# Performance work log

Hardware: AMD Instinct MI355X
Metric: run time of the kernel (lower is better)

Reference implementation:

```python
import jax, jax.numpy as jnp
import numpy as np

N_QUBIT = 20
N_LAYER = 50
FEAT = 128
BATCH = 128
N_NODES = BATCH * N_QUBIT * (N_LAYER + 1)  # 130560
N_EDGES = 524288
VOCAB = N_QUBIT * (N_LAYER + 1) + 1  # 1021
NEG_SLOPE = 0.01


def setup_inputs() -> dict:
    key = jax.random.key(0)
    ks = jax.random.split(key, 32)
    s = 0.05
    x = jax.random.randint(ks[0], (N_NODES,), 0, VOCAB, dtype=jnp.int64 if jax.config.read('jax_enable_x64') else jnp.int32)
    edge_index = jax.random.randint(ks[1], (2, N_EDGES), 0, N_NODES, dtype=x.dtype)
    emb = (jax.random.normal(ks[2], (VOCAB, FEAT), jnp.float32) * s).at[0].set(0.0)  # padding_idx=0
    gcn_w = jax.random.normal(ks[3], (5, FEAT, FEAT), jnp.float32) * s
    gcn_b = jnp.zeros((5, FEAT), jnp.float32)
    mlp_dims = [(2 * FEAT, 2 * FEAT), (2 * FEAT, FEAT), (FEAT, FEAT), (FEAT, FEAT // 2), (FEAT // 2, FEAT // 2), (FEAT // 2, 1)]
    mlp = {}
    for i, (din, dout) in enumerate(mlp_dims):
        mlp[f'mw{i}'] = jax.random.normal(ks[4 + i], (din, dout), jnp.float32) * s
        mlp[f'mb{i}'] = jnp.zeros((dout,), jnp.float32)
    return dict(x=x, edge_index=edge_index, emb=emb, gcn_w=gcn_w, gcn_b=gcn_b, **mlp)


def _leaky(v):
    return jnp.where(v >= 0, v, NEG_SLOPE * v)


def _gcn(h, src, dst, W, b):
    # PyG GCNConv: h' = D^-1/2 (A+I) D^-1/2 (h W) + b, flow src -> dst
    n = h.shape[0]
    hw = h @ W
    loops = jnp.arange(n, dtype=src.dtype)
    s2 = jnp.concatenate([src, loops])
    d2 = jnp.concatenate([dst, loops])
    deg = jax.ops.segment_sum(jnp.ones(s2.shape[0], hw.dtype), d2, num_segments=n)
    dinv = jnp.where(deg > 0, jax.lax.rsqrt(deg), 0.0)
    norm = dinv[s2] * dinv[d2]  # [E+N]
    out = jax.ops.segment_sum(hw[s2] * norm[:, None], d2, num_segments=n)
    return out + b


def reference(x, edge_index, emb, gcn_w, gcn_b, mw0, mb0, mw1, mb1, mw2, mb2, mw3, mb3, mw4, mb4, mw5, mb5):
    src, dst = edge_index[0], edge_index[1]
    h = emb[x]  # [N, f]
    for i in range(4):
        h = _leaky(_gcn(h, src, dst, gcn_w[i], gcn_b[i])) + h
    h = _gcn(h, src, dst, gcn_w[4], gcn_b[4]) + h
    n, f = N_QUBIT, FEAT
    h = h.reshape(-1, n * (N_LAYER + 1), f)[:, :n, :]  # [B, n, f]
    b = h.shape[0]
    # cartesian pairs (i, j): concat(h_i, h_j) -> [B, n, n, 2f]
    xi = jnp.broadcast_to(h[:, :, None, :], (b, n, n, f))
    xj = jnp.broadcast_to(h[:, None, :, :], (b, n, n, f))
    p = jnp.concatenate([xi, xj], axis=-1)
    p = _leaky(p @ mw0 + mb0)
    p = _leaky(p @ mw1 + mb1)
    p = _leaky(p @ mw2 + mb2)
    p = _leaky(p @ mw3 + mb3)
    p = _leaky(p @ mw4 + mb4)
    p = (p @ mw5 + mb5)[..., 0]  # [B, n, n]
    p = (p + jnp.swapaxes(p, -1, -2)) / 2
    return p.reshape(-1, n * n)
```

## Files before the change

kernel.cpp:

```cpp
#include <hip/hip_runtime.h>
#include <hip/hip_bf16.h>

#define NQ 20
#define NLAY 51
#define FEAT 128
#define BATCH 128
#define NN (BATCH * NQ * NLAY)
#define NE 524288
#define NPAIR (BATCH * NQ * NQ)
#define NB (NN / 256)
#define VOCAB 1021

typedef _Float16 half8 __attribute__((ext_vector_type(8)));
typedef float floatx4 __attribute__((ext_vector_type(4)));
typedef unsigned int uint;

__device__ __forceinline__ float lrelu(float v) { return v >= 0.f ? v : 0.01f * v; }

__device__ __forceinline__ uint packhl(float v) {
    _Float16 h = (_Float16)v;
    _Float16 l = (_Float16)(v - (float)h);
    union { _Float16 f; unsigned short u; } hb, lb;
    hb.f = h; lb.f = l;
    return (uint)hb.u | ((uint)lb.u << 16);
// ... 17 lines not shown
    int e = blockIdx.x * 256 + threadIdx.x;
    atomicAdd(&cnt[dst[e]], 1);
}

__global__ void k_offsets(const int* __restrict__ cnt, const int* __restrict__ x,
                          int* __restrict__ offs, float* __restrict__ dinv,
                          int4* __restrict__ meta, int* __restrict__ cursor,
                          int* __restrict__ flag1, int* __restrict__ idmap) {
    __shared__ int sm[256];
    __shared__ int sbase;
    int t = threadIdx.x, g = blockIdx.x * 256 + t;
    int v = cnt[g];
    sm[t] = v;
    __syncthreads();
    for (int s = 1; s < 256; s <<= 1) {
        int add = (t >= s) ? sm[t - s] : 0;
        __syncthreads();
        sm[t] += add;
        __syncthreads();
    }
    if (t == 255) sbase = atomicAdd(cursor, sm[255]);
    __syncthreads();
    int off = sbase + sm[t] - v;
    float di = rsqrtf((float)(v + 1));
    offs[g] = off;
    dinv[g] = di;
    meta[g] = make_int4(off, v, __float_as_int(di), x[g]);
    if (g % (NQ * NLAY) < NQ) flag1[g] = 1;
    if (g < 1024) idmap[g] = min(g, VOCAB - 1);
}

__global__ void k_fill(const int* __restrict__ src, const int* __restrict__ dst,
                       const int* __restrict__ offs, int* __restrict__ fill,
                       const float* __restrict__ dinv, const int* __restrict__ x,
                       int2* __restrict__ csre, int2* __restrict__ csre0,
                       int* __restrict__ flag1) {
    int e = blockIdx.x * 256 + threadIdx.x;
    int d = dst[e];
    int s = src[e];
    int pos = offs[d] + atomicAdd(&fill[d], 1);
    int wb = __float_as_int(dinv[s] * dinv[d]);
    csre[pos] = make_int2(s, wb);
    csre0[pos] = make_int2(x[s], wb);
    if (d % (NQ * NLAY) < NQ) flag1[s] = 1;
}

__global__ void k_s1pass(const int* __restrict__ flagI, const int4* __restrict__ meta,
                         const int2* __restrict__ csre, int* __restrict__ cur,
                         int* __restrict__ listO, int4* __restrict__ recO,
                         int* __restrict__ flagO) {
    __shared__ int sm[256];
    __shared__ int sbase;
    int t = threadIdx.x, g = blockIdx.x * 256 + t;
    int v = flagI[g];
    sm[t] = v;
    __syncthreads();
    for (int s = 1; s < 256; s <<= 1) {
        int add = (t >= s) ? sm[t - s] : 0;
        __syncthreads();
        sm[t] += add;
        __syncthreads();
    }
    if (t == 255) sbase = atomicAdd(cur, sm[255]);
    __syncthreads();
    if (v) {
        int slot = sbase + sm[t] - 1;
        listO[slot] = g;
        int4 m = meta[g];
        float di = __int_as_float(m.z);
        int dc = min(m.y, 6);
        int2 eb[6];
#pragma unroll
        for (int j = 0; j < 6; j++) eb[j] = (j < dc) ? csre[m.x + j] : make_int2(0, 0);
        int4* r = recO + (size_t)slot * 4;
        r[0] = make_int4(g + 1, m.y, __float_as_int(di * di), m.x);
        r[1] = make_int4(eb[0].x, eb[0].y, eb[1].x, eb[1].y);
        r[2] = make_int4(eb[2].x, eb[2].y, eb[3].x, eb[3].y);
        r[3] = make_int4(eb[4].x, eb[4].y, eb[5].x, eb[5].y);
        if (flagO) {
            flagO[g] = 1;
            for (int e = 0; e < m.y; e++) flagO[csre[m.x + e].x] = 1;
        }
    }
}

#define OFF_GCN 0
#define OFF_P0  81920
#define OFF_M1  147456
#define OFF_M2  180224
#define OFF_M3  196608
#define OFF_M4  204800
#define TS_TOTAL 208896

__global__ void k_tsplit_all(const float* __restrict__ gw, const float* __restrict__ mw0,
                             const float* __restrict__ mw1, const float* __restrict__ mw2,
                             const float* __restrict__ mw3, const float* __restrict__ mw4,
                             _Float16* __restrict__ hi, _Float16* __restrict__ lo) {
    int idx = blockIdx.x * 256 + threadIdx.x;
    const float* src;
    int K, N, rel;
    bool p0 = false;
    if (idx < OFF_P0) {
        int L = (idx - OFF_GCN) >> 14; rel = (idx - OFF_GCN) & 16383;
        src = gw + L * 16384; K = 128; N = 128;
    } else if (idx < OFF_M1) {
        rel = idx - OFF_P0; src = mw0; K = 128; N = 512; p0 = true;
    } else if (idx < OFF_M2) {
        rel = idx - OFF_M1;  src = mw1; K = 256; N = 128;
    } else if (idx < OFF_M3) {
        rel = idx - OFF_M2;  src = mw2; K = 128; N = 128;
    } else if (idx < OFF_M4) {
        rel = idx - OFF_M3;  src = mw3; K = 128; N = 64;
    } else {
        rel = idx - OFF_M4;  src = mw4; K = 64;  N = 64;
    }
    int kblks = K >> 5;
    int j = rel & 7;
    int lane = (rel >> 3) & 63;
    int t2 = rel >> 9;
    int kblk = t2 % kblks;
    int ntile = t2 / kblks;
    int col = ntile * 16 + (lane & 15);
    int k = kblk * 32 + ((lane >> 4) << 3) + j;
    float f;
    if (p0) {
        f = (col < 256) ? src[k * 256 + col] : src[(k + 128) * 256 + (col - 256)];
    } else {
        f = src[k * N + col];
    }
    _Float16 h = (_Float16)f;
    hi[idx] = h;
    lo[idx] = (_Float16)(f - (float)h);
}

template <int NT_N, bool LEAKY, bool BIAS, bool P0SPLIT, bool FUSEA, bool GATHA, bool LISTM>
__launch_bounds__(256, 2)
__global__ void hgemm(const float* __restrict__ A,
                      const float* __restrict__ FA, const float* __restrict__ FB,
                      const _Float16* __restrict__ Bh, const _Float16* __restrict__ Bl,
                      const float* __restrict__ bias,
                      float* __restrict__ C, float* __restrict__ C2,
                      int N, int K, const int* __restrict__ gmap,
                      const int* __restrict__ listm) {
    if (LISTM) {
        if ((unsigned)listm[blockIdx.x * 128] >= (unsigned)NN) return;
    }
    const int KB = K >> 5;
    const int lane = threadIdx.x & 63;
    const int wid = threadIdx.x >> 6;
    const int lm = lane & 15, lq = lane >> 4;
    const int m0 = blockIdx.x * 128 + wid * 32;
    const int n0t = blockIdx.y * NT_N;

    const float* arow[2];
    const float* brow[2];
#pragma unroll
    for (int mt = 0; mt < 2; mt++) {
        int row = m0 + mt * 16 + lm;
        if (FUSEA) {
            int b = row / (NQ * NQ);
            int rr = row - b * (NQ * NQ);
            int i = rr / NQ;
            int j = rr - i * NQ;
            arow[mt] = FA + (size_t)(b * NQ + i) * 256;
            brow[mt] = FB + (size_t)(b * NQ + j) * 256;
        } else if (GATHA) {
// ... 14 lines not shown
        for (int nt = 0; nt < NT_N; nt++) acc[mt][nt] = (floatx4)0.f;

    for (int kb = 0; kb < KB; kb++) {
        const int k0 = kb * 32 + lq * 8;
        half8 ahi[2], alo[2];
#pragma unroll
        for (int mt = 0; mt < 2; mt++) {
            floatx4 av0, av1;
            if (FUSEA) {
                floatx4 fa0 = *(const floatx4*)(arow[mt] + k0);
                floatx4 fa1 = *(const floatx4*)(arow[mt] + k0 + 4);
                floatx4 fb0 = *(const floatx4*)(brow[mt] + k0);
                floatx4 fb1 = *(const floatx4*)(brow[mt] + k0 + 4);
#pragma unroll
                for (int q = 0; q < 4; q++) {
                    av0[q] = lrelu(fa0[q] + fb0[q]);
                    av1[q] = lrelu(fa1[q] + fb1[q]);
                }
            } else {
                av0 = *(const floatx4*)(arow[mt] + k0);
                av1 = *(const floatx4*)(arow[mt] + k0 + 4);
            }
#pragma unroll
            for (int q = 0; q < 4; q++) {
                _Float16 h0 = (_Float16)av0[q];
                ahi[mt][q] = h0;
                alo[mt][q] = (_Float16)(av0[q] - (float)h0);
                _Float16 h1 = (_Float16)av1[q];
                ahi[mt][4 + q] = h1;
                alo[mt][4 + q] = (_Float16)(av1[q] - (float)h1);
            }
        }
#pragma unroll
        for (int nt = 0; nt < NT_N; nt++) {
            size_t boff = (((size_t)(n0t + nt) * KB + kb) * 64 + lane) * 8;
            half8 bhi = *(const half8*)(Bh + boff);
            half8 blo = *(const half8*)(Bl + boff);
#pragma unroll
            for (int mt = 0; mt < 2; mt++) {
                acc[mt][nt] = __builtin_amdgcn_mfma_f32_16x16x32_f16(ahi[mt], bhi, acc[mt][nt], 0, 0, 0);
                acc[mt][nt] = __builtin_amdgcn_mfma_f32_16x16x32_f16(ahi[mt], blo, acc[mt][nt], 0, 0, 0);
                acc[mt][nt] = __builtin_amdgcn_mfma_f32_16x16x32_f16(alo[mt], bhi, acc[mt][nt], 0, 0, 0);
            }
        }
    }

    int strow[2][4];
    bool svalid[2][4];
#pragma unroll
    for (int mt = 0; mt < 2; mt++)
#pragma unroll
        for (int r = 0; r < 4; r++) {
            int mlog = m0 + mt * 16 + lq * 4 + r;
            if (LISTM) {
                int sr = listm[mlog];
                svalid[mt][r] = (unsigned)sr < (unsigned)NN;
                strow[mt][r] = svalid[mt][r] ? sr : 0;
            } else {
                svalid[mt][r] = true;
                strow[mt][r] = mlog;
            }
        }

#pragma unroll
    for (int nt = 0; nt < NT_N; nt++) {
        int col = (n0t + nt) * 16 + lm;
        float bv = (BIAS || P0SPLIT) ? bias[col < 256 ? col : 0] : 0.f;
#pragma unroll
        for (int mt = 0; mt < 2; mt++) {
#pragma unroll
            for (int r = 0; r < 4; r++) {
                if (!svalid[mt][r]) continue;
                int row = strow[mt][r];
                float val = acc[mt][nt][r];
                if (P0SPLIT) {
                    if (col < 256) C[(size_t)row * 256 + col] = val + bv;
                    else C2[(size_t)row * 256 + col - 256] = val;
                } else {
                    if (BIAS) val += bv;
                    if (LEAKY) val = lrelu(val);
                    C[(size_t)row * N + col] = val;
                }
            }
        }
    }
}

template <int KB, int NT>
__device__ __forceinline__ void pair_stage(uint (*__restrict__ X)[132],
                                           const _Float16* __restrict__ Bh,
                                           const _Float16* __restrict__ Bl,
                                           const float* __restrict__ bias,
                                           int srow, int lane) {
    const int lm = lane & 15, lq = lane >> 4;
    floatx4 acc[NT];
#pragma unroll
    for (int nt = 0; nt < NT; nt++) acc[nt] = (floatx4)0.f;
#pragma unroll
    for (int kb = 0; kb < KB; kb++) {
        const int k0 = kb * 32 + lq * 8;
        uint4 pa = *(const uint4*)&X[srow + lm][k0];
        uint4 pb = *(const uint4*)&X[srow + lm][k0 + 4];
        half8 ahi, alo;
        unpack8(pa, pb, ahi, alo);
#pragma unroll
        for (int nt = 0; nt < NT; nt++) {
            size_t boff = (((size_t)nt * KB + kb) * 64 + lane) * 8;
            half8 bhi = *(const half8*)(Bh + boff);
            half8 blo = *(const half8*)(Bl + boff);
            acc[nt] = __builtin_amdgcn_mfma_f32_16x16x32_f16(ahi, bhi, acc[nt], 0, 0, 0);
            acc[nt] = __builtin_amdgcn_mfma_f32_16x16x32_f16(ahi, blo, acc[nt], 0, 0, 0);
            acc[nt] = __builtin_amdgcn_mfma_f32_16x16x32_f16(alo, bhi, acc[nt], 0, 0, 0);
        }
    }
#pragma unroll
    for (int nt = 0; nt < NT; nt++) {
        int col = nt * 16 + lm;
        float bv = bias[col];
#pragma unroll
        for (int r = 0; r < 4; r++) {
            X[srow + lq * 4 + r][col] = packhl(lrelu(acc[nt][r] + bv));
        }
    }
}

__launch_bounds__(256, 4)
__global__ void k_pair(const float* __restrict__ FA, const float* __restrict__ FB,
                       const _Float16* __restrict__ bth, const _Float16* __restrict__ btl,
                       const float* __restrict__ mb1, const float* __restrict__ mb2,
                       const float* __restrict__ mb3, const float* __restrict__ mb4,
                       const float* __restrict__ mw5, const float* __restrict__ mb5,
                       float* __restrict__ sbuf) {
    __shared__ uint X[64][132];
    const int lane = threadIdx.x & 63;
    const int wid = threadIdx.x >> 6;
    const int lm = lane & 15, lq = lane >> 4;
    const int srow = wid * 16;
    const int rbase = blockIdx.x * 64;

    {
        const int grow = rbase + srow + lm;
        int b = grow / (NQ * NQ);
        int rr = grow - b * (NQ * NQ);
        int i = rr / NQ;
        int j = rr - i * NQ;
        const float* arow = FA + (size_t)(b * NQ + i) * 256;
        const float* brow = FB + (size_t)(b * NQ + j) * 256;
        const _Float16* Bh = bth + OFF_M1;
        const _Float16* Bl = btl + OFF_M1;
        floatx4 acc[8];
#pragma unroll
        for (int nt = 0; nt < 8; nt++) acc[nt] = (floatx4)0.f;
        const int KB = 8;
#pragma unroll
        for (int kb = 0; kb < KB; kb++) {
            const int k0 = kb * 32 + lq * 8;
            floatx4 fa0 = *(const floatx4*)(arow + k0);
            floatx4 fa1 = *(const floatx4*)(arow + k0 + 4);
            floatx4 fb0 = *(const floatx4*)(brow + k0);
            floatx4 fb1 = *(const floatx4*)(brow + k0 + 4);
            half8 ahi, alo;
#pragma unroll
            for (int q = 0; q < 4; q++) {
                float v0 = lrelu(fa0[q] + fb0[q]);
                float v1 = lrelu(fa1[q] + fb1[q]);
                _Float16 h0 = (_Float16)v0;
// ... 49 lines not shown
        if (part == 0) sbuf[rbase + row] = s + mb5[0];
    }
}

__global__ void k_sym(const float* __restrict__ sbuf, float* __restrict__ out) {
    int p = blockIdx.x * 256 + threadIdx.x;
    int b = p / (NQ * NQ);
    int rr = p - b * (NQ * NQ);
    int i = rr / NQ, j = rr - i * NQ;
    float a = sbuf[p];
    float c = sbuf[b * (NQ * NQ) + j * NQ + i];
    out[p] = 0.5f * (a + c);
}

__global__ void k_agg0(const float* __restrict__ embW, const float* __restrict__ emb,
                       float* __restrict__ h,
                       const int4* __restrict__ meta, const int2* __restrict__ csre0,
                       const float* __restrict__ bias) {
    int tid = threadIdx.x;
    int sl = tid & 31;
    int p = blockIdx.x * 8 + (tid >> 5);
    int n0 = p * 2, n1 = n0 + 1;
    int4 m0 = meta[n0], m1 = meta[n1];
    float di0 = __int_as_float(m0.z), di1 = __int_as_float(m1.z);
    int off0 = m0.x, deg0 = m0.y;
    int off1 = m1.x, deg1 = m1.y;
    float4 v0 = ((const float4*)(embW + (size_t)m0.w * FEAT))[sl];
    float4 v1 = ((const float4*)(embW + (size_t)m1.w * FEAT))[sl];
    float4 ho0 = ((const float4*)(emb + (size_t)m0.w * FEAT))[sl];
    float4 ho1 = ((const float4*)(emb + (size_t)m1.w * FEAT))[sl];
    float s20 = di0 * di0, s21 = di1 * di1;
    float a0x = v0.x * s20, a0y = v0.y * s20, a0z = v0.z * s20, a0w = v0.w * s20;
    float a1x = v1.x * s21, a1y = v1.y * s21, a1z = v1.z * s21, a1w = v1.w * s21;
    int d0c = max(deg0 - 1, 0), d1c = max(deg1 - 1, 0);
    int dm = max(deg0, deg1);
    for (int e = 0; e < dm; e += 4) {
        int2 e00 = csre0[off0 + min(e,     d0c)];
        int2 e01 = csre0[off0 + min(e + 1, d0c)];
        int2 e02 = csre0[off0 + min(e + 2, d0c)];
        int2 e03 = csre0[off0 + min(e + 3, d0c)];
        int2 e10 = csre0[off1 + min(e,     d1c)];
        int2 e11 = csre0[off1 + min(e + 1, d1c)];
        int2 e12 = csre0[off1 + min(e + 2, d1c)];
        int2 e13 = csre0[off1 + min(e + 3, d1c)];
        float4 u00 = ((const float4*)(embW + (size_t)e00.x * FEAT))[sl];
        float4 u01 = ((const float4*)(embW + (size_t)e01.x * FEAT))[sl];
        float4 u02 = ((const float4*)(embW + (size_t)e02.x * FEAT))[sl];
        float4 u03 = ((const float4*)(embW + (size_t)e03.x * FEAT))[sl];
        float4 u10 = ((const float4*)(embW + (size_t)e10.x * FEAT))[sl];
        float4 u11 = ((const float4*)(embW + (size_t)e11.x * FEAT))[sl];
        float4 u12 = ((const float4*)(embW + (size_t)e12.x * FEAT))[sl];
        float4 u13 = ((const float4*)(embW + (size_t)e13.x * FEAT))[sl];
        float w00 = (e     < deg0) ? __int_as_float(e00.y) : 0.f;
        float w01 = (e + 1 < deg0) ? __int_as_float(e01.y) : 0.f;
        float w02 = (e + 2 < deg0) ? __int_as_float(e02.y) : 0.f;
        float w03 = (e + 3 < deg0) ? __int_as_float(e03.y) : 0.f;
        float w10 = (e     < deg1) ? __int_as_float(e10.y) : 0.f;
        float w11 = (e + 1 < deg1) ? __int_as_float(e11.y) : 0.f;
        float w12 = (e + 2 < deg1) ? __int_as_float(e12.y) : 0.f;
        float w13 = (e + 3 < deg1) ? __int_as_float(e13.y) : 0.f;
        a0x += u00.x * w00 + u01.x * w01 + u02.x * w02 + u03.x * w03;
        a0y += u00.y * w00 + u01.y * w01 + u02.y * w02 + u03.y * w03;
        a0z += u00.z * w00 + u01.z * w01 + u02.z * w02 + u03.z * w03;
        a0w += u00.w * w00 + u01.w * w01 + u02.w * w02 + u03.w * w03;
        a1x += u10.x * w10 + u11.x * w11 + u12.x * w12 + u13.x * w13;
        a1y += u10.y * w10 + u11.y * w11 + u12.y * w12 + u13.y * w13;
        a1z += u10.z * w10 + u11.z * w11 + u12.z * w12 + u13.z * w13;
        a1w += u10.w * w10 + u11.w * w11 + u12.w * w12 + u13.w * w13;
    }
    float4 bv = ((const float4*)bias)[sl];
    float4 r0, r1;
    r0.x = lrelu(a0x + bv.x) + ho0.x;
    r0.y = lrelu(a0y + bv.y) + ho0.y;
    r0.z = lrelu(a0z + bv.z) + ho0.z;
    r0.w = lrelu(a0w + bv.w) + ho0.w;
    r1.x = lrelu(a1x + bv.x) + ho1.x;
    r1.y = lrelu(a1y + bv.y) + ho1.y;
    r1.z = lrelu(a1z + bv.z) + ho1.z;
    r1.w = lrelu(a1w + bv.w) + ho1.w;
    ((float4*)(h + (size_t)n0 * FEAT))[sl] = r0;
    ((float4*)(h + (size_t)n1 * FEAT))[sl] = r1;
}

__global__ void k_agg(const float* __restrict__ hw, float* __restrict__ h,
                      const int4* __restrict__ rec, const int2* __restrict__ csre,
                      const int* __restrict__ cntp, const float* __restrict__ bias) {
    int lcnt = *cntp;
    if (blockIdx.x * 16 >= lcnt) return;
    int tid = threadIdx.x;
    int sl = tid & 31;
    int p = blockIdx.x * 8 + (tid >> 5);
    int p0i = p * 2, p1i = p0i + 1;
    bool val0 = p0i < lcnt, val1 = p1i < lcnt;
    const int4* r0p = rec + (size_t)(val0 ? p0i : 0) * 4;
    const int4* r1p = rec + (size_t)(val1 ? p1i : 0) * 4;
    int4 hd0 = r0p[0], ea0 = r0p[1], eb0 = r0p[2], ec0 = r0p[3];
    int4 hd1 = r1p[0], ea1 = r1p[1], eb1 = r1p[2], ec1 = r1p[3];
    int n0 = hd0.x - 1;
    int n1 = hd1.x - 1;
    float s20 = __int_as_float(hd0.z), s21 = __int_as_float(hd1.z);
    const float4* hw4 = (const float4*)hw;
    float4 v0  = hw4[(size_t)n0 * 32 + sl];
    float4 v1  = hw4[(size_t)n1 * 32 + sl];
    float4 u00 = hw4[(size_t)ea0.x * 32 + sl];
    float4 u01 = hw4[(size_t)ea0.z * 32 + sl];
    float4 u02 = hw4[(size_t)eb0.x * 32 + sl];
    float4 u03 = hw4[(size_t)eb0.z * 32 + sl];
    float4 u04 = hw4[(size_t)ec0.x * 32 + sl];
    float4 u05 = hw4[(size_t)ec0.z * 32 + sl];
    float4 u10 = hw4[(size_t)ea1.x * 32 + sl];
    float4 u11 = hw4[(size_t)ea1.z * 32 + sl];
    float4 u12 = hw4[(size_t)eb1.x * 32 + sl];
    float4 u13 = hw4[(size_t)eb1.z * 32 + sl];
    float4 u14 = hw4[(size_t)ec1.x * 32 + sl];
    float4 u15 = hw4[(size_t)ec1.z * 32 + sl];
    float4 ho0 = ((const float4*)h)[(size_t)n0 * 32 + sl];
    float4 ho1 = ((const float4*)h)[(size_t)n1 * 32 + sl];
    float w00 = __int_as_float(ea0.y), w01 = __int_as_float(ea0.w);
    float w02 = __int_as_float(eb0.y), w03 = __int_as_float(eb0.w);
    float w04 = __int_as_float(ec0.y), w05 = __int_as_float(ec0.w);
    float w10 = __int_as_float(ea1.y), w11 = __int_as_float(ea1.w);
    float w12 = __int_as_float(eb1.y), w13 = __int_as_float(eb1.w);
    float w14 = __int_as_float(ec1.y), w15 = __int_as_float(ec1.w);
    float a0x = v0.x * s20 + u00.x * w00 + u01.x * w01 + u02.x * w02 + u03.x * w03 + u04.x * w04 + u05.x * w05;
    float a0y = v0.y * s20 + u00.y * w00 + u01.y * w01 + u02.y * w02 + u03.y * w03 + u04.y * w04 + u05.y * w05;
    float a0z = v0.z * s20 + u00.z * w00 + u01.z * w01 + u02.z * w02 + u03.z * w03 + u04.z * w04 + u05.z * w05;
    float a0w = v0.w * s20 + u00.w * w00 + u01.w * w01 + u02.w * w02 + u03.w * w03 + u04.w * w04 + u05.w * w05;
    float a1x = v1.x * s21 + u10.x * w10 + u11.x * w11 + u12.x * w12 + u13.x * w13 + u14.x * w14 + u15.x * w15;
    float a1y = v1.y * s21 + u10.y * w10 + u11.y * w11 + u12.y * w12 + u13.y * w13 + u14.y * w14 + u15.y * w15;
    float a1z = v1.z * s21 + u10.z * w10 + u11.z * w11 + u12.z * w12 + u13.z * w13 + u14.z * w14 + u15.z * w15;
    float a1w = v1.w * s21 + u10.w * w10 + u11.w * w11 + u12.w * w12 + u13.w * w13 + u14.w * w14 + u15.w * w15;
    int deg0 = val0 ? hd0.y : 0, deg1 = val1 ? hd1.y : 0;
    int dm = max(deg0, deg1);
    if (dm > 6) {
        int off0 = hd0.w, off1 = hd1.w;
        int d0c = max(deg0 - 1, 0), d1c = max(deg1 - 1, 0);
        for (int e = 6; e < dm; e += 6) {
            int2 e00 = csre[off0 + min(e,     d0c)];
            int2 e01 = csre[off0 + min(e + 1, d0c)];
            int2 e02 = csre[off0 + min(e + 2, d0c)];
            int2 e03 = csre[off0 + min(e + 3, d0c)];
            int2 e04 = csre[off0 + min(e + 4, d0c)];
            int2 e05 = csre[off0 + min(e + 5, d0c)];
            int2 e10 = csre[off1 + min(e,     d1c)];
            int2 e11 = csre[off1 + min(e + 1, d1c)];
            int2 e12 = csre[off1 + min(e + 2, d1c)];
            int2 e13 = csre[off1 + min(e + 3, d1c)];
            int2 e14 = csre[off1 + min(e + 4, d1c)];
            int2 e15 = csre[off1 + min(e + 5, d1c)];
            float4 x00 = hw4[(size_t)e00.x * 32 + sl];
            float4 x01 = hw4[(size_t)e01.x * 32 + sl];
            float4 x02 = hw4[(size_t)e02.x * 32 + sl];
            float4 x03 = hw4[(size_t)e03.x * 32 + sl];
            float4 x04 = hw4[(size_t)e04.x * 32 + sl];
            float4 x05 = hw4[(size_t)e05.x * 32 + sl];
            float4 x10 = hw4[(size_t)e10.x * 32 + sl];
            float4 x11 = hw4[(size_t)e11.x * 32 + sl];
            float4 x12 = hw4[(size_t)e12.x * 32 + sl];
            float4 x13 = hw4[(size_t)e13.x * 32 + sl];
            float4 x14 = hw4[(size_t)e14.x * 32 + sl];
            float4 x15 = hw4[(size_t)e15.x * 32 + sl];
            float q00 = (e     < deg0) ? __int_as_float(e00.y) : 0.f;
            float q01 = (e + 1 < deg0) ? __int_as_float(e01.y) : 0.f;
            float q02 = (e + 2 < deg0) ? __int_as_float(e02.y) : 0.f;
            float q03 = (e + 3 < deg0) ? __int_as_float(e03.y) : 0.f;
            float q04 = (e + 4 < deg0) ? __int_as_float(e04.y) : 0.f;
            float q05 = (e + 5 < deg0) ? __int_as_float(e05.y) : 0.f;
            float q10 = (e     < deg1) ? __int_as_float(e10.y) : 0.f;
            float q11 = (e + 1 < deg1) ? __int_as_float(e11.y) : 0.f;
            float q12 = (e + 2 < deg1) ? __int_as_float(e12.y) : 0.f;
            float q13 = (e + 3 < deg1) ? __int_as_float(e13.y) : 0.f;
            float q14 = (e + 4 < deg1) ? __int_as_float(e14.y) : 0.f;
            float q15 = (e + 5 < deg1) ? __int_as_float(e15.y) : 0.f;
            a0x += x00.x * q00 + x01.x * q01 + x02.x * q02 + x03.x * q03 + x04.x * q04 + x05.x * q05;
            a0y += x00.y * q00 + x01.y * q01 + x02.y * q02 + x03.y * q03 + x04.y * q04 + x05.y * q05;
            a0z += x00.z * q00 + x01.z * q01 + x02.z * q02 + x03.z * q03 + x04.z * q04 + x05.z * q05;
            a0w += x00.w * q00 + x01.w * q01 + x02.w * q02 + x03.w * q03 + x04.w * q04 + x05.w * q05;
            a1x += x10.x * q10 + x11.x * q11 + x12.x * q12 + x13.x * q13 + x14.x * q14 + x15.x * q15;
            a1y += x10.y * q10 + x11.y * q11 + x12.y * q12 + x13.y * q13 + x14.y * q14 + x15.y * q15;
            a1z += x10.z * q10 + x11.z * q11 + x12.z * q12 + x13.z * q13 + x14.z * q14 + x15.z * q15;
            a1w += x10.w * q10 + x11.w * q11 + x12.w * q12 + x13.w * q13 + x14.w * q14 + x15.w * q15;
        }
    }
    float4 bv = ((const float4*)bias)[sl];
    float4 r0, r1;
    r0.x = lrelu(a0x + bv.x) + ho0.x;
    r0.y = lrelu(a0y + bv.y) + ho0.y;
    r0.z = lrelu(a0z + bv.z) + ho0.z;
    r0.w = lrelu(a0w + bv.w) + ho0.w;
    r1.x = lrelu(a1x + bv.x) + ho1.x;
    r1.y = lrelu(a1y + bv.y) + ho1.y;
    r1.z = lrelu(a1z + bv.z) + ho1.z;
    r1.w = lrelu(a1w + bv.w) + ho1.w;
    if (val0) ((float4*)(h + (size_t)n0 * FEAT))[sl] = r0;
    if (val1) ((float4*)(h + (size_t)n1 * FEAT))[sl] = r1;
}

__global__ void k_aggq(const float* __restrict__ hw, const float* __restrict__ h,
                       const int4* __restrict__ meta, const int2* __restrict__ csre,
                       const float* __restrict__ gbias, float* __restrict__ hq) {
    int tid = threadIdx.x;
    int sl = tid & 31;
    int q = blockIdx.x * 8 + (tid >> 5);
    int b = q / NQ, i = q - b * NQ;
    int node = b * (NQ * NLAY) + i;
    int4 m = meta[node];
    float di = __int_as_float(m.z);
    int off = m.x, deg = m.y;
    float s2 = di * di;
    float4 v = ((const float4*)(hw + (size_t)node * FEAT))[sl];
    float ax = v.x * s2, ay = v.y * s2, az = v.z * s2, aw = v.w * s2;
    int dc = max(deg - 1, 0);
    for (int e = 0; e < deg; e += 4) {
        int2 e0 = csre[off + min(e,     dc)];
        int2 e1 = csre[off + min(e + 1, dc)];
        int2 e2 = csre[off + min(e + 2, dc)];
        int2 e3 = csre[off + min(e + 3, dc)];
        float4 u0 = ((const float4*)(hw + (size_t)e0.x * FEAT))[sl];
        float4 u1 = ((const float4*)(hw + (size_t)e1.x * FEAT))[sl];
        float4 u2 = ((const float4*)(hw + (size_t)e2.x * FEAT))[sl];
        float4 u3 = ((const float4*)(hw + (size_t)e3.x * FEAT))[sl];
        float w0 = (e     < deg) ? __int_as_float(e0.y) : 0.f;
        float w1 = (e + 1 < deg) ? __int_as_float(e1.y) : 0.f;
        float w2 = (e + 2 < deg) ? __int_as_float(e2.y) : 0.f;
        float w3 = (e + 3 < deg) ? __int_as_float(e3.y) : 0.f;
        ax += u0.x * w0 + u1.x * w1 + u2.x * w2 + u3.x * w3;
        ay += u0.y * w0 + u1.y * w1 + u2.y * w2 + u3.y * w3;
        az += u0.z * w0 + u1.z * w1 + u2.z * w2 + u3.z * w3;
        aw += u0.w * w0 + u1.w * w1 + u2.w * w2 + u3.w * w3;
    }
    float4 bv = ((const float4*)gbias)[sl];
    float4 ho = ((const float4*)(h + (size_t)node * FEAT))[sl];
    ((float4*)(hq + (size_t)q * FEAT))[sl] =
        make_float4(ax + bv.x + ho.x, ay + bv.y + ho.y, az + bv.z + ho.z, aw + bv.w + ho.w);
}

extern "C" void kernel_launch(void* const* d_in, const int* in_sizes, int n_in,
                              void* d_out, int out_size, void* d_ws, size_t ws_size,
                              hipStream_t stream) {
    const int* x = (const int*)d_in[0];
    const int* ei = (const int*)d_in[1];
    const int* e_src = ei;
    const int* e_dst = ei + NE;
    const float* emb = (const float*)d_in[2];
    const float* gw = (const float*)d_in[3];
    const float* gb = (const float*)d_in[4];
    const float* mw0 = (const float*)d_in[5];
    const float* mb0 = (const float*)d_in[6];
    const float* mw1 = (const float*)d_in[7];
    const float* mb1 = (const float*)d_in[8];
    const float* mw2 = (const float*)d_in[9];
    const float* mb2 = (const float*)d_in[10];
    const float* mw3 = (const float*)d_in[11];
    const float* mb3 = (const float*)d_in[12];
    const float* mw4 = (const float*)d_in[13];
    const float* mb4 = (const float*)d_in[14];
    const float* mw5 = (const float*)d_in[15];
    const float* mb5 = (const float*)d_in[16];
    float* out = (float*)d_out;

    float* wsf = (float*)d_ws;
    size_t o = 0;
    const size_t HSZ = (size_t)NN * FEAT;
    float* h  = wsf + o; o += HSZ;
    float* hw = wsf + o; o += HSZ;
    int* cnt   = (int*)(wsf + o); o += NN;
    int* fill  = (int*)(wsf + o); o += NN;
    int* flag1 = (int*)(wsf + o); o += NN;
    int* flag2 = (int*)(wsf + o); o += NN;
    int* flag3 = (int*)(wsf + o); o += NN;
    int* curs  = (int*)(wsf + o); o += 16;
    int* list1 = (int*)(wsf + o); o += NN;
    int* list2 = (int*)(wsf + o); o += NN;
    int* list3 = (int*)(wsf + o); o += NN;
    int* offs = (int*)(wsf + o); o += NN;
    float* dinv = wsf + o; o += NN;
    int4* meta = (int4*)(wsf + o); o += 4 * (size_t)NN;
    int2* csre  = (int2*)(wsf + o); o += 2 * (size_t)(NE + 8);
    int2* csre0 = (int2*)(wsf + o); o += 2 * (size_t)(NE + 8);
    int* idmap = (int*)(wsf + o); o += 1024;
    float* embW = wsf + o; o += (size_t)1024 * FEAT;
    float* hq = wsf + o; o += (size_t)BATCH * NQ * FEAT;
    float* Abuf = wsf + o; o += (size_t)BATCH * NQ * 256;
    float* Bbuf = wsf + o; o += (size_t)BATCH * NQ * 256;
    int4* rec1 = (int4*)(wsf + o); o += 16 * (size_t)NN;
    int4* rec2 = (int4*)(wsf + o); o += 16 * (size_t)NN;
    int4* rec3 = (int4*)(wsf + o); o += 16 * (size_t)NN;
    _Float16* bt_hi = (_Float16*)(wsf + o); o += (TS_TOTAL + 2) / 2;
    _Float16* bt_lo = (_Float16*)(wsf + o); o += (TS_TOTAL + 2) / 2;
    float* sbuf = hw;

    k_tsplit_all<<<TS_TOTAL / 256, 256, 0, stream>>>(gw, mw0, mw1, mw2, mw3, mw4, bt_hi, bt_lo);

    hipMemsetAsync(cnt, 0, (5 * NN + 16) * sizeof(int), stream);
    hipMemsetAsync(list1, 0xFF, 3 * NN * sizeof(int), stream);
    hipMemsetAsync(csre + NE, 0, 8 * sizeof(int2), stream);
    hipMemsetAsync(csre0 + NE, 0, 8 * sizeof(int2), stream);
    k_count<<<NE / 256, 256, 0, stream>>>(e_dst, cnt);
    k_offsets<<<NB, 256, 0, stream>>>(cnt, x, offs, dinv, meta, curs + 0, flag1, idmap);
    k_fill<<<NE / 256, 256, 0, stream>>>(e_src, e_dst, offs, fill, dinv, x, csre, csre0, flag1);
    k_s1pass<<<NB, 256, 0, stream>>>(flag1, meta, csre, curs + 1, list1, rec1, flag2);
    k_s1pass<<<NB, 256, 0, stream>>>(flag2, meta, csre, curs + 2, list2, rec2, flag3);
    k_s1pass<<<NB, 256, 0, stream>>>(flag3, meta, csre, curs + 3, list3, rec3, nullptr);

    hgemm<1, false, false, false, false, true, false><<<dim3(8, 8), 256, 0, stream>>>(
        emb, nullptr, nullptr, bt_hi + OFF_GCN, bt_lo + OFF_GCN,
        nullptr, embW, nullptr, FEAT, FEAT, idmap, nullptr);
    k_agg0<<<NN / 16, 256, 0, stream>>>(embW, emb, h, meta, csre0, gb + 0 * FEAT);

    hgemm<8, false, false, false, false, false, false><<<dim3(NN / 128, 1), 256, 0, stream>>>(
        h, nullptr, nullptr, bt_hi + OFF_GCN + 1 * 16384, bt_lo + OFF_GCN + 1 * 16384,
        nullptr, hw, nullptr, FEAT, FEAT, nullptr, nullptr);
    k_agg<<<NN / 16, 256, 0, stream>>>(hw, h, rec3, csre, curs + 3, gb + 1 * FEAT);

    hgemm<8, false, false, false, false, false, true><<<dim3(NN / 128, 1), 256, 0, stream>>>(
        h, nullptr, nullptr, bt_hi + OFF_GCN + 2 * 16384, bt_lo + OFF_GCN + 2 * 16384,
        nullptr, hw, nullptr, FEAT, FEAT, nullptr, list3);
    k_agg<<<NN / 16, 256, 0, stream>>>(hw, h, rec2, csre, curs + 2, gb + 2 * FEAT);

    hgemm<8, false, false, false, false, false, true><<<dim3(NN / 128, 1), 256, 0, stream>>>(
        h, nullptr, nullptr, bt_hi + OFF_GCN + 3 * 16384, bt_lo + OFF_GCN + 3 * 16384,
        nullptr, hw, nullptr, FEAT, FEAT, nullptr, list2);
    k_agg<<<NN / 16, 256, 0, stream>>>(hw, h, rec1, csre, curs + 1, gb + 3 * FEAT);

    hgemm<8, false, false, false, false, false, true><<<dim3(NN / 128, 1), 256, 0, stream>>>(
        h, nullptr, nullptr, bt_hi + OFF_GCN + 4 * 16384, bt_lo + OFF_GCN + 4 * 16384,
        nullptr, hw, nullptr, FEAT, FEAT, nullptr, list1);
    k_aggq<<<(BATCH * NQ) / 8, 256, 0, stream>>>(hw, h, meta, csre,
                                                 gb + 4 * (size_t)FEAT, hq);

    hgemm<2, false, false, true, false, false, false><<<dim3(20, 16), 256, 0, stream>>>(
        hq, nullptr, nullptr, bt_hi + OFF_P0, bt_lo + OFF_P0, mb0, Abuf, Bbuf, 512, 128,
        nullptr, nullptr);
    k_pair<<<NPAIR / 64, 256, 0, stream>>>(Abuf, Bbuf, bt_hi, bt_lo,
                                           mb1, mb2, mb3, mb4, mw5, mb5, sbuf);
    k_sym<<<NPAIR / 256, 256, 0, stream>>>(sbuf, out);
}
```

Measured before the change: 470.5 us.

## Fuse GCN aggregation with weight GEMM by aggregating features before transform

Reorders each GCN layer from A·(H·W) to (A·H)·W. The normalized neighbor aggregation is gathered directly into a shared-memory tile of split-fp16 values, and the 128x128 weight multiply is then done with MFMA in the same kernel. Bias, leaky ReLU and the residual add are applied in the epilogue, and h/hw act as ping-pong buffers. The separate per-layer hgemm launches, the full-size hw intermediate round trip and the list memset are removed, and a small rec0 record table drives the final query-node layer. In exchange each block does gathers and a GEMM together, which uses more LDS and registers and may lower occupancy.

```diff
diff --git a/kernel.cpp b/kernel.cpp
--- a/kernel.cpp
+++ b/kernel.cpp
@@ -123,6 +123,25 @@
             for (int e = 0; e < m.y; e++) flagO[csre[m.x + e].x] = 1;
         }
     }
+}
+
+__global__ void k_rec0(const int4* __restrict__ meta, const int2* __restrict__ csre,
+                       int4* __restrict__ rec0) {
+    int q = blockIdx.x * 256 + threadIdx.x;
+    if (q >= BATCH * NQ) return;
+    int b = q / NQ, i = q - b * NQ;
+    int node = b * (NQ * NLAY) + i;
+    int4 m = meta[node];
+    float di = __int_as_float(m.z);
+    int dc = min(m.y, 6);
+    int2 eb[6];
+#pragma unroll
+    for (int j = 0; j < 6; j++) eb[j] = (j < dc) ? csre[m.x + j] : make_int2(0, 0);
+    int4* r = rec0 + (size_t)q * 4;
+    r[0] = make_int4(node + 1, m.y, __float_as_int(di * di), m.x);
+    r[1] = make_int4(eb[0].x, eb[0].y, eb[1].x, eb[1].y);
+    r[2] = make_int4(eb[2].x, eb[2].y, eb[3].x, eb[3].y);
+    r[3] = make_int4(eb[4].x, eb[4].y, eb[5].x, eb[5].y);
 }
 
 #define OFF_GCN 0
@@ -303,6 +322,169 @@
                     C[(size_t)row * N + col] = val;
                 }
             }
+        }
+    }
+}
+
+template <bool LEAKY, bool FINAL>
+__launch_bounds__(256, 4)
+__global__ void k_lagg(const float* __restrict__ in, float* __restrict__ outp,
+                       const int4* __restrict__ rec, const int2* __restrict__ csre,
+                       const int* __restrict__ cntp, int fixcnt,
+                       const _Float16* __restrict__ Bh, const _Float16* __restrict__ Bl,
+                       const float* __restrict__ bias) {
+    int lcnt = cntp ? *cntp : fixcnt;
+    int sbase = blockIdx.x * 64;
+    if (sbase >= lcnt) return;
+    __shared__ uint X[64][132];
+    int tid = threadIdx.x;
+    int sl = tid & 31;
+    int grp = tid >> 5;
+    const float4* in4 = (const float4*)in;
+#pragma unroll 1
+    for (int pass = 0; pass < 4; pass++) {
+        int lrow0 = pass * 16 + grp * 2;
+        int p0i = sbase + lrow0, p1i = p0i + 1;
+        bool val0 = p0i < lcnt, val1 = p1i < lcnt;
+        const int4* r0p = rec + (size_t)(val0 ? p0i : 0) * 4;
+        const int4* r1p = rec + (size_t)(val1 ? p1i : 0) * 4;
+        int4 hd0 = r0p[0], ea0 = r0p[1], eb0 = r0p[2], ec0 = r0p[3];
+        int4 hd1 = r1p[0], ea1 = r1p[1], eb1 = r1p[2], ec1 = r1p[3];
+        int n0 = hd0.x - 1;
+        int n1 = hd1.x - 1;
+        float s20 = __int_as_float(hd0.z), s21 = __int_as_float(hd1.z);
+        float4 v0  = in4[(size_t)n0 * 32 + sl];
+        float4 v1  = in4[(size_t)n1 * 32 + sl];
+        float4 u00 = in4[(size_t)ea0.x * 32 + sl];
+        float4 u01 = in4[(size_t)ea0.z * 32 + sl];
+        float4 u02 = in4[(size_t)eb0.x * 32 + sl];
+        float4 u03 = in4[(size_t)eb0.z * 32 + sl];
+        float4 u04 = in4[(size_t)ec0.x * 32 + sl];
+        float4 u05 = in4[(size_t)ec0.z * 32 + sl];
+        float4 u10 = in4[(size_t)ea1.x * 32 + sl];
+        float4 u11 = in4[(size_t)ea1.z * 32 + sl];
+        float4 u12 = in4[(size_t)eb1.x * 32 + sl];
+        float4 u13 = in4[(size_t)eb1.z * 32 + sl];
+        float4 u14 = in4[(size_t)ec1.x * 32 + sl];
+        float4 u15 = in4[(size_t)ec1.z * 32 + sl];
+        float w00 = __int_as_float(ea0.y), w01 = __int_as_float(ea0.w);
+        float w02 = __int_as_float(eb0.y), w03 = __int_as_float(eb0.w);
+        float w04 = __int_as_float(ec0.y), w05 = __int_as_float(ec0.w);
+        float w10 = __int_as_float(ea1.y), w11 = __int_as_float(ea1.w);
+        float w12 = __int_as_float(eb1.y), w13 = __int_as_float(eb1.w);
+        float w14 = __int_as_float(ec1.y), w15 = __int_as_float(ec1.w);
+        float a0x = v0.x * s20 + u00.x * w00 + u01.x * w01 + u02.x * w02 + u03.x * w03 + u04.x * w04 + u05.x * w05;
+        float a0y = v0.y * s20 + u00.y * w00 + u01.y * w01 + u02.y * w02 + u03.y * w03 + u04.y * w04 + u05.y * w05;
+        float a0z = v0.z * s20 + u00.z * w00 + u01.z * w01 + u02.z * w02 + u03.z * w03 + u04.z * w04 + u05.z * w05;
+        float a0w = v0.w * s20 + u00.w * w00 + u01.w * w01 + u02.w * w02 + u03.w * w03 + u04.w * w04 + u05.w * w05;
+        float a1x = v1.x * s21 + u10.x * w10 + u11.x * w11 + u12.x * w12 + u13.x * w13 + u14.x * w14 + u15.x * w15;
+        float a1y = v1.y * s21 + u10.y * w10 + u11.y * w11 + u12.y * w12 + u13.y * w13 + u14.y * w14 + u15.y * w15;
+        float a1z = v1.z * s21 + u10.z * w10 + u11.z * w11 + u12.z * w12 + u13.z * w13 + u14.z * w14 + u15.z * w15;
+        float a1w = v1.w * s21 + u10.w * w10 + u11.w * w11 + u12.w * w12 + u13.w * w13 + u14.w * w14 + u15.w * w15;
+        int deg0 = val0 ? hd0.y : 0, deg1 = val1 ? hd1.y : 0;
+        int dm = max(deg0, deg1);
+        if (dm > 6) {
+            int off0 = hd0.w, off1 = hd1.w;
+            int d0c = max(deg0 - 1, 0), d1c = max(deg1 - 1, 0);
+            for (int e = 6; e < dm; e += 6) {
+                int2 e00 = csre[off0 + min(e,     d0c)];
+                int2 e01 = csre[off0 + min(e + 1, d0c)];
+                int2 e02 = csre[off0 + min(e + 2, d0c)];
+                int2 e03 = csre[off0 + min(e + 3, d0c)];
+                int2 e04 = csre[off0 + min(e + 4, d0c)];
+                int2 e05 = csre[off0 + min(e + 5, d0c)];
+                int2 e10 = csre[off1 + min(e,     d1c)];
+                int2 e11 = csre[off1 + min(e + 1, d1c)];
+                int2 e12 = csre[off1 + min(e + 2, d1c)];
+                int2 e13 = csre[off1 + min(e + 3, d1c)];
+                int2 e14 = csre[off1 + min(e + 4, d1c)];
+                int2 e15 = csre[off1 + min(e + 5, d1c)];
+                float4 x00 = in4[(size_t)e00.x * 32 + sl];
+                float4 x01 = in4[(size_t)e01.x * 32 + sl];
+                float4 x02 = in4[(size_t)e02.x * 32 + sl];
+                float4 x03 = in4[(size_t)e03.x * 32 + sl];
+                float4 x04 = in4[(size_t)e04.x * 32 + sl];
+                float4 x05 = in4[(size_t)e05.x * 32 + sl];
+                float4 x10 = in4[(size_t)e10.x * 32 + sl];
+                float4 x11 = in4[(size_t)e11.x * 32 + sl];
+                float4 x12 = in4[(size_t)e12.x * 32 + sl];
+                float4 x13 = in4[(size_t)e13.x * 32 + sl];
+                float4 x14 = in4[(size_t)e14.x * 32 + sl];
+                float4 x15 = in4[(size_t)e15.x * 32 + sl];
+                float q00 = (e     < deg0) ? __int_as_float(e00.y) : 0.f;
+                float q01 = (e + 1 < deg0) ? __int_as_float(e01.y) : 0.f;
+                float q02 = (e + 2 < deg0) ? __int_as_float(e02.y) : 0.f;
+                float q03 = (e + 3 < deg0) ? __int_as_float(e03.y) : 0.f;
+                float q04 = (e + 4 < deg0) ? __int_as_float(e04.y) : 0.f;
+                float q05 = (e + 5 < deg0) ? __int_as_float(e05.y) : 0.f;
+                float q10 = (e     < deg1) ? __int_as_float(e10.y) : 0.f;
+                float q11 = (e + 1 < deg1) ? __int_as_float(e11.y) : 0.f;
+                float q12 = (e + 2 < deg1) ? __int_as_float(e12.y) : 0.f;
+                float q13 = (e + 3 < deg1) ? __int_as_float(e13.y) : 0.f;
+                float q14 = (e + 4 < deg1) ? __int_as_float(e14.y) : 0.f;
+                float q15 = (e + 5 < deg1) ? __int_as_float(e15.y) : 0.f;
+                a0x += x00.x * q00 + x01.x * q01 + x02.x * q02 + x03.x * q03 + x04.x * q04 + x05.x * q05;
+                a0y += x00.y * q00 + x01.y * q01 + x02.y * q02 + x03.y * q03 + x04.y * q04 + x05.y * q05;
+                a0z += x00.z * q00 + x01.z * q01 + x02.z * q02 + x03.z * q03 + x04.z * q04 + x05.z * q05;
+                a0w += x00.w * q00 + x01.w * q01 + x02.w * q02 + x03.w * q03 + x04.w * q04 + x05.w * q05;
+                a1x += x10.x * q10 + x11.x * q11 + x12.x * q12 + x13.x * q13 + x14.x * q14 + x15.x * q15;
+                a1y += x10.y * q10 + x11.y * q11 + x12.y * q12 + x13.y * q13 + x14.y * q14 + x15.y * q15;
+                a1z += x10.z * q10 + x11.z * q11 + x12.z * q12 + x13.z * q13 + x14.z * q14 + x15.z * q15;
+                a1w += x10.w * q10 + x11.w * q11 + x12.w * q12 + x13.w * q13 + x14.w * q14 + x15.w * q15;
+            }
+        }
+        *(uint4*)&X[lrow0][sl * 4] =
+            make_uint4(packhl(a0x), packhl(a0y), packhl(a0z), packhl(a0w));
+        *(uint4*)&X[lrow0 + 1][sl * 4] =
+            make_uint4(packhl(a1x), packhl(a1y), packhl(a1z), packhl(a1w));
+    }
+    __syncthreads();
+    const int lane = tid & 63;
+    const int wid = tid >> 6;
+    const int lm = lane & 15, lq = lane >> 4;
+    const int srow = wid * 16;
+    floatx4 acc[8];
+#pragma unroll
+    for (int nt = 0; nt < 8; nt++) acc[nt] = (floatx4)0.f;
+#pragma unroll
+    for (int kb = 0; kb < 4; kb++) {
+        const int k0 = kb * 32 + lq * 8;
+        uint4 pa = *(const uint4*)&X[srow + lm][k0];
+        uint4 pb = *(const uint4*)&X[srow + lm][k0 + 4];
+        half8 ahi, alo;
+        unpack8(pa, pb, ahi, alo);
+#pragma unroll
+        for (int nt = 0; nt < 8; nt++) {
+            size_t boff = (((size_t)nt * 4 + kb) * 64 + lane) * 8;
+            half8 bhi = *(const half8*)(Bh + boff);
+            half8 blo = *(const half8*)(Bl + boff);
+            acc[nt] = __builtin_amdgcn_mfma_f32_16x16x32_f16(ahi, bhi, acc[nt], 0, 0, 0);
+            acc[nt] = __builtin_amdgcn_mfma_f32_16x16x32_f16(ahi, blo, acc[nt], 0, 0, 0);
+            acc[nt] = __builtin_amdgcn_mfma_f32_16x16x32_f16(alo, bhi, acc[nt], 0, 0, 0);
+        }
+    }
+    int nodes[4];
+    bool sval[4];
+#pragma unroll
+    for (int r = 0; r < 4; r++) {
+        int slot = sbase + srow + lq * 4 + r;
+        sval[r] = slot < lcnt;
+        nodes[r] = sval[r] ? (rec[(size_t)slot * 4].x - 1) : 0;
+    }
+#pragma unroll
+    for (int nt = 0; nt < 8; nt++) {
+        int col = nt * 16 + lm;
+        float bv = bias[col];
+#pragma unroll
+        for (int r = 0; r < 4; r++) {
+            if (!sval[r]) continue;
+            float val = acc[nt][r] + bv;
+            if (LEAKY) val = lrelu(val);
+            val += in[(size_t)nodes[r] * FEAT + col];
+            if (FINAL)
+                outp[(size_t)(sbase + srow + lq * 4 + r) * FEAT + col] = val;
+            else
+                outp[(size_t)nodes[r] * FEAT + col] = val;
         }
     }
 }
@@ -518,159 +700,6 @@
     ((float4*)(h + (size_t)n1 * FEAT))[sl] = r1;
 }
 
-__global__ void k_agg(const float* __restrict__ hw, float* __restrict__ h,
-                      const int4* __restrict__ rec, const int2* __restrict__ csre,
-                      const int* __restrict__ cntp, const float* __restrict__ bias) {
-    int lcnt = *cntp;
-    if (blockIdx.x * 16 >= lcnt) return;
-    int tid = threadIdx.x;
-    int sl = tid & 31;
-    int p = blockIdx.x * 8 + (tid >> 5);
-    int p0i = p * 2, p1i = p0i + 1;
-    bool val0 = p0i < lcnt, val1 = p1i < lcnt;
-    const int4* r0p = rec + (size_t)(val0 ? p0i : 0) * 4;
-    const int4* r1p = rec + (size_t)(val1 ? p1i : 0) * 4;
-    int4 hd0 = r0p[0], ea0 = r0p[1], eb0 = r0p[2], ec0 = r0p[3];
-    int4 hd1 = r1p[0], ea1 = r1p[1], eb1 = r1p[2], ec1 = r1p[3];
-    int n0 = hd0.x - 1;
-    int n1 = hd1.x - 1;
-    float s20 = __int_as_float(hd0.z), s21 = __int_as_float(hd1.z);
-    const float4* hw4 = (const float4*)hw;
-    float4 v0  = hw4[(size_t)n0 * 32 + sl];
-    float4 v1  = hw4[(size_t)n1 * 32 + sl];
-    float4 u00 = hw4[(size_t)ea0.x * 32 + sl];
-    float4 u01 = hw4[(size_t)ea0.z * 32 + sl];
-    float4 u02 = hw4[(size_t)eb0.x * 32 + sl];
-    float4 u03 = hw4[(size_t)eb0.z * 32 + sl];
-    float4 u04 = hw4[(size_t)ec0.x * 32 + sl];
-    float4 u05 = hw4[(size_t)ec0.z * 32 + sl];
-    float4 u10 = hw4[(size_t)ea1.x * 32 + sl];
-    float4 u11 = hw4[(size_t)ea1.z * 32 + sl];
-    float4 u12 = hw4[(size_t)eb1.x * 32 + sl];
-    float4 u13 = hw4[(size_t)eb1.z * 32 + sl];
-    float4 u14 = hw4[(size_t)ec1.x * 32 + sl];
-    float4 u15 = hw4[(size_t)ec1.z * 32 + sl];
-    float4 ho0 = ((const float4*)h)[(size_t)n0 * 32 + sl];
-    float4 ho1 = ((const float4*)h)[(size_t)n1 * 32 + sl];
-    float w00 = __int_as_float(ea0.y), w01 = __int_as_float(ea0.w);
-    float w02 = __int_as_float(eb0.y), w03 = __int_as_float(eb0.w);
-    float w04 = __int_as_float(ec0.y), w05 = __int_as_float(ec0.w);
-    float w10 = __int_as_float(ea1.y), w11 = __int_as_float(ea1.w);
-    float w12 = __int_as_float(eb1.y), w13 = __int_as_float(eb1.w);
-    float w14 = __int_as_float(ec1.y), w15 = __int_as_float(ec1.w);
-    float a0x = v0.x * s20 + u00.x * w00 + u01.x * w01 + u02.x * w02 + u03.x * w03 + u04.x * w04 + u05.x * w05;
-    float a0y = v0.y * s20 + u00.y * w00 + u01.y * w01 + u02.y * w02 + u03.y * w03 + u04.y * w04 + u05.y * w05;
-    float a0z = v0.z * s20 + u00.z * w00 + u01.z * w01 + u02.z * w02 + u03.z * w03 + u04.z * w04 + u05.z * w05;
-    float a0w = v0.w * s20 + u00.w * w00 + u01.w * w01 + u02.w * w02 + u03.w * w03 + u04.w * w04 + u05.w * w05;
-    float a1x = v1.x * s21 + u10.x * w10 + u11.x * w11 + u12.x * w12 + u13.x * w13 + u14.x * w14 + u15.x * w15;
-    float a1y = v1.y * s21 + u10.y * w10 + u11.y * w11 + u12.y * w12 + u13.y * w13 + u14.y * w14 + u15.y * w15;
-    float a1z = v1.z * s21 + u10.z * w10 + u11.z * w11 + u12.z * w12 + u13.z * w13 + u14.z * w14 + u15.z * w15;
-    float a1w = v1.w * s21 + u10.w * w10 + u11.w * w11 + u12.w * w12 + u13.w * w13 + u14.w * w14 + u15.w * w15;
-    int deg0 = val0 ? hd0.y : 0, deg1 = val1 ? hd1.y : 0;
-    int dm = max(deg0, deg1);
-    if (dm > 6) {
-        int off0 = hd0.w, off1 = hd1.w;
-        int d0c = max(deg0 - 1, 0), d1c = max(deg1 - 1, 0);
-        for (int e = 6; e < dm; e += 6) {
-            int2 e00 = csre[off0 + min(e,     d0c)];
-            int2 e01 = csre[off0 + min(e + 1, d0c)];
-            int2 e02 = csre[off0 + min(e + 2, d0c)];
-            int2 e03 = csre[off0 + min(e + 3, d0c)];
-            int2 e04 = csre[off0 + min(e + 4, d0c)];
-            int2 e05 = csre[off0 + min(e + 5, d0c)];
-            int2 e10 = csre[off1 + min(e,     d1c)];
-            int2 e11 = csre[off1 + min(e + 1, d1c)];
-            int2 e12 = csre[off1 + min(e + 2, d1c)];
-            int2 e13 = csre[off1 + min(e + 3, d1c)];
-            int2 e14 = csre[off1 + min(e + 4, d1c)];
-            int2 e15 = csre[off1 + min(e + 5, d1c)];
-            float4 x00 = hw4[(size_t)e00.x * 32 + sl];
-            float4 x01 = hw4[(size_t)e01.x * 32 + sl];
-            float4 x02 = hw4[(size_t)e02.x * 32 + sl];
-            float4 x03 = hw4[(size_t)e03.x * 32 + sl];
-            float4 x04 = hw4[(size_t)e04.x * 32 + sl];
-            float4 x05 = hw4[(size_t)e05.x * 32 + sl];
-            float4 x10 = hw4[(size_t)e10.x * 32 + sl];
-            float4 x11 = hw4[(size_t)e11.x * 32 + sl];
-            float4 x12 = hw4[(size_t)e12.x * 32 + sl];
-            float4 x13 = hw4[(size_t)e13.x * 32 + sl];
-            float4 x14 = hw4[(size_t)e14.x * 32 + sl];
-            float4 x15 = hw4[(size_t)e15.x * 32 + sl];
-            float q00 = (e     < deg0) ? __int_as_float(e00.y) : 0.f;
-            float q01 = (e + 1 < deg0) ? __int_as_float(e01.y) : 0.f;
-            float q02 = (e + 2 < deg0) ? __int_as_float(e02.y) : 0.f;
-            float q03 = (e + 3 < deg0) ? __int_as_float(e03.y) : 0.f;
-            float q04 = (e + 4 < deg0) ? __int_as_float(e04.y) : 0.f;
-            float q05 = (e + 5 < deg0) ? __int_as_float(e05.y) : 0.f;
-            float q10 = (e     < deg1) ? __int_as_float(e10.y) : 0.f;
-            float q11 = (e + 1 < deg1) ? __int_as_float(e11.y) : 0.f;
-            float q12 = (e + 2 < deg1) ? __int_as_float(e12.y) : 0.f;
-            float q13 = (e + 3 < deg1) ? __int_as_float(e13.y) : 0.f;
-            float q14 = (e + 4 < deg1) ? __int_as_float(e14.y) : 0.f;
-            float q15 = (e + 5 < deg1) ? __int_as_float(e15.y) : 0.f;
-            a0x += x00.x * q00 + x01.x * q01 + x02.x * q02 + x03.x * q03 + x04.x * q04 + x05.x * q05;
-            a0y += x00.y * q00 + x01.y * q01 + x02.y * q02 + x03.y * q03 + x04.y * q04 + x05.y * q05;
-            a0z += x00.z * q00 + x01.z * q01 + x02.z * q02 + x03.z * q03 + x04.z * q04 + x05.z * q05;
-            a0w += x00.w * q00 + x01.w * q01 + x02.w * q02 + x03.w * q03 + x04.w * q04 + x05.w * q05;
-            a1x += x10.x * q10 + x11.x * q11 + x12.x * q12 + x13.x * q13 + x14.x * q14 + x15.x * q15;
-            a1y += x10.y * q10 + x11.y * q11 + x12.y * q12 + x13.y * q13 + x14.y * q14 + x15.y * q15;
-            a1z += x10.z * q10 + x11.z * q11 + x12.z * q12 + x13.z * q13 + x14.z * q14 + x15.z * q15;
-            a1w += x10.w * q10 + x11.w * q11 + x12.w * q12 + x13.w * q13 + x14.w * q14 + x15.w * q15;
-        }
-    }
-    float4 bv = ((const float4*)bias)[sl];
-    float4 r0, r1;
-    r0.x = lrelu(a0x + bv.x) + ho0.x;
-    r0.y = lrelu(a0y + bv.y) + ho0.y;
-    r0.z = lrelu(a0z + bv.z) + ho0.z;
-    r0.w = lrelu(a0w + bv.w) + ho0.w;
-    r1.x = lrelu(a1x + bv.x) + ho1.x;
-    r1.y = lrelu(a1y + bv.y) + ho1.y;
-    r1.z = lrelu(a1z + bv.z) + ho1.z;
-    r1.w = lrelu(a1w + bv.w) + ho1.w;
-    if (val0) ((float4*)(h + (size_t)n0 * FEAT))[sl] = r0;
-    if (val1) ((float4*)(h + (size_t)n1 * FEAT))[sl] = r1;
-}
-
-__global__ void k_aggq(const float* __restrict__ hw, const float* __restrict__ h,
-                       const int4* __restrict__ meta, const int2* __restrict__ csre,
-                       const float* __restrict__ gbias, float* __restrict__ hq) {
-    int tid = threadIdx.x;
-    int sl = tid & 31;
-    int q = blockIdx.x * 8 + (tid >> 5);
-    int b = q / NQ, i = q - b * NQ;
-    int node = b * (NQ * NLAY) + i;
-    int4 m = meta[node];
-    float di = __int_as_float(m.z);
-    int off = m.x, deg = m.y;
-    float s2 = di * di;
-    float4 v = ((const float4*)(hw + (size_t)node * FEAT))[sl];
-    float ax = v.x * s2, ay = v.y * s2, az = v.z * s2, aw = v.w * s2;
-    int dc = max(deg - 1, 0);
-    for (int e = 0; e < deg; e += 4) {
-        int2 e0 = csre[off + min(e,     dc)];
-        int2 e1 = csre[off + min(e + 1, dc)];
-        int2 e2 = csre[off + min(e + 2, dc)];
-        int2 e3 = csre[off + min(e + 3, dc)];
-        float4 u0 = ((const float4*)(hw + (size_t)e0.x * FEAT))[sl];
-        float4 u1 = ((const float4*)(hw + (size_t)e1.x * FEAT))[sl];
-        float4 u2 = ((const float4*)(hw + (size_t)e2.x * FEAT))[sl];
-        float4 u3 = ((const float4*)(hw + (size_t)e3.x * FEAT))[sl];
-        float w0 = (e     < deg) ? __int_as_float(e0.y) : 0.f;
-        float w1 = (e + 1 < deg) ? __int_as_float(e1.y) : 0.f;
-        float w2 = (e + 2 < deg) ? __int_as_float(e2.y) : 0.f;
-        float w3 = (e + 3 < deg) ? __int_as_float(e3.y) : 0.f;
-        ax += u0.x * w0 + u1.x * w1 + u2.x * w2 + u3.x * w3;
-        ay += u0.y * w0 + u1.y * w1 + u2.y * w2 + u3.y * w3;
-        az += u0.z * w0 + u1.z * w1 + u2.z * w2 + u3.z * w3;
-        aw += u0.w * w0 + u1.w * w1 + u2.w * w2 + u3.w * w3;
-    }
-    float4 bv = ((const float4*)gbias)[sl];
-    float4 ho = ((const float4*)(h + (size_t)node * FEAT))[sl];
-    ((float4*)(hq + (size_t)q * FEAT))[sl] =
-        make_float4(ax + bv.x + ho.x, ay + bv.y + ho.y, az + bv.z + ho.z, aw + bv.w + ho.w);
-}
-
 extern "C" void kernel_launch(void* const* d_in, const int* in_sizes, int n_in,
                               void* d_out, int out_size, void* d_ws, size_t ws_size,
                               hipStream_t stream) {
@@ -722,6 +751,7 @@
     int4* rec1 = (int4*)(wsf + o); o += 16 * (size_t)NN;
     int4* rec2 = (int4*)(wsf + o); o += 16 * (size_t)NN;
     int4* rec3 = (int4*)(wsf + o); o += 16 * (size_t)NN;
+    int4* rec0 = (int4*)(wsf + o); o += 16 * (size_t)(BATCH * NQ);
     _Float16* bt_hi = (_Float16*)(wsf + o); o += (TS_TOTAL + 2) / 2;
     _Float16* bt_lo = (_Float16*)(wsf + o); o += (TS_TOTAL + 2) / 2;
     float* sbuf = hw;
@@ -729,12 +759,12 @@
     k_tsplit_all<<<TS_TOTAL / 256, 256, 0, stream>>>(gw, mw0, mw1, mw2, mw3, mw4, bt_hi, bt_lo);
 
     hipMemsetAsync(cnt, 0, (5 * NN + 16) * sizeof(int), stream);
-    hipMemsetAsync(list1, 0xFF, 3 * NN * sizeof(int), stream);
     hipMemsetAsync(csre + NE, 0, 8 * sizeof(int2), stream);
     hipMemsetAsync(csre0 + NE, 0, 8 * sizeof(int2), stream);
     k_count<<<NE / 256, 256, 0, stream>>>(e_dst, cnt);
     k_offsets<<<NB, 256, 0, stream>>>(cnt, x, offs, dinv, meta, curs + 0, flag1, idmap);
     k_fill<<<NE / 256, 256, 0, stream>>>(e_src, e_dst, offs, fill, dinv, x, csre, csre0, flag1);
+    k_rec0<<<(BATCH * NQ + 255) / 256, 256, 0, stream>>>(meta, csre, rec0);
     k_s1pass<<<NB, 256, 0, stream>>>(flag1, meta, csre, curs + 1, list1, rec1, flag2);
     k_s1pass<<<NB, 256, 0, stream>>>(flag2, meta, csre, curs + 2, list2, rec2, flag3);
     k_s1pass<<<NB, 256, 0, stream>>>(flag3, meta, csre, curs + 3, list3, rec3, nullptr);
@@ -744,26 +774,18 @@
         nullptr, embW, nullptr, FEAT, FEAT, idmap, nullptr);
     k_agg0<<<NN / 16, 256, 0, stream>>>(embW, emb, h, meta, csre0, gb + 0 * FEAT);
 
-    hgemm<8, false, false, false, false, false, false><<<dim3(NN / 128, 1), 256, 0, stream>>>(
-        h, nullptr, nullptr, bt_hi + OFF_GCN + 1 * 16384, bt_lo + OFF_GCN + 1 * 16384,
-        nullptr, hw, nullptr, FEAT, FEAT, nullptr, nullptr);
-    k_agg<<<NN / 16, 256, 0, stream>>>(hw, h, rec3, csre, curs + 3, gb + 1 * FEAT);
-
-    hgemm<8, false, false, false, false, false, true><<<dim3(NN / 128, 1), 256, 0, stream>>>(
-        h, nullptr, nullptr, bt_hi + OFF_GCN + 2 * 16384, bt_lo + OFF_GCN + 2 * 16384,
-        nullptr, hw, nullptr, FEAT, FEAT, nullptr, list3);
-    k_agg<<<NN / 16, 256, 0, stream>>>(hw, h, rec2, csre, curs + 2, gb + 2 * FEAT);
-
-    hgemm<8, false, false, false, false, false, true><<<dim3(NN / 128, 1), 256, 0, stream>>>(
-        h, nullptr, nullptr, bt_hi + OFF_GCN + 3 * 16384, bt_lo + OFF_GCN + 3 * 16384,
-        nullptr, hw, nullptr, FEAT, FEAT, nullptr, list2);
-    k_agg<<<NN / 16, 256, 0, stream>>>(hw, h, rec1, csre, curs + 1, gb + 3 * FEAT);
-
-    hgemm<8, false, false, false, false, false, true><<<dim3(NN / 128, 1), 256, 0, stream>>>(
-        h, nullptr, nullptr, bt_hi + OFF_GCN + 4 * 16384, bt_lo + OFF_GCN + 4 * 16384,
-        nullptr, hw, nullptr, FEAT, FEAT, nullptr, list1);
-    k_aggq<<<(BATCH * NQ) / 8, 256, 0, stream>>>(hw, h, meta, csre,
-                                                 gb + 4 * (size_t)FEAT, hq);
+    k_lagg<true, false><<<NN / 64, 256, 0, stream>>>(
+        h, hw, rec3, csre, curs + 3, 0,
+        bt_hi + OFF_GCN + 1 * 16384, bt_lo + OFF_GCN + 1 * 16384, gb + 1 * FEAT);
+    k_lagg<true, false><<<NN / 64, 256, 0, stream>>>(
+        hw, h, rec2, csre, curs + 2, 0,
+        bt_hi + OFF_GCN + 2 * 16384, bt_lo + OFF_GCN + 2 * 16384, gb + 2 * FEAT);
+    k_lagg<true, false><<<NN / 64, 256, 0, stream>>>(
+        h, hw, rec1, csre, curs + 1, 0,
+        bt_hi + OFF_GCN + 3 * 16384, bt_lo + OFF_GCN + 3 * 16384, gb + 3 * FEAT);
+    k_lagg<false, true><<<(BATCH * NQ) / 64, 256, 0, stream>>>(
+        hw, hq, rec0, csre, nullptr, BATCH * NQ,
+        bt_hi + OFF_GCN + 4 * 16384, bt_lo + OFF_GCN + 4 * 16384, gb + 4 * FEAT);
 
     hgemm<2, false, false, true, false, false, false><<<dim3(20, 16), 256, 0, stream>>>(
         hq, nullptr, nullptr, bt_hi + OFF_P0, bt_lo + OFF_P0, mb0, Abuf, Bbuf, 512, 128,
```

After: 447.1 us. 5.0% less time.
